# Kernel optimization log

Hardware: AMD Instinct MI355X
Metric: run time of the kernel (lower is better)

## Reference

```python
import jax, jax.numpy as jnp
import numpy as np

N_NODES = 10000
N_EDGES = 160000
M0, M1, M2 = 16, 8, 4            # multiplicities of 0e / 1o / 2e node channels
D_HID = 64                        # radial MLP hidden width
N_BASIS = 4                       # bessel radial basis size
N_STEPS = 3                       # message passing steps
R_MAX = 2.0                       # bessel cutoff
S_CNT = (M0+1)+(M1+1)+(M2+1)      # 31 scalar channels of edge TP output
V_CNT = (M0+1)+3*(M1+1)+2*(M2+1)  # 54 vector channels
T_CNT = (M0+1)+2*(M1+1)+3*(M2+1)  # 50 l=2 channels
NUM_IRREPS = S_CNT+V_CNT+T_CNT    # 135 = radial-MLP output size

def _basis():
    # orthonormal basis of traceless symmetric 3x3 matrices, SH ordering (xy, yz, 3z2-r2, xz, x2-y2)
    B = np.zeros((5,3,3), np.float32); r2 = 1/np.sqrt(2.); r6 = 1/np.sqrt(6.)
    B[0,0,1]=B[0,1,0]=r2
    B[1,1,2]=B[1,2,1]=r2
    B[2]=np.diag([-r6,-r6,2*r6])
    B[3,0,2]=B[3,2,0]=r2
    B[4]=np.diag([r2,-r2,0.])
    return B
_B = jnp.asarray(_basis())

def _eps():
    e = np.zeros((3,3,3), np.float32)
    e[0,1,2]=e[1,2,0]=e[2,0,1]=1.; e[0,2,1]=e[2,1,0]=e[1,0,2]=-1.
    return e
_EPS = jnp.asarray(_eps())

def to_mat(a): return jnp.einsum('...k,kij->...ij', a, _B)
def to5(M):    return jnp.einsum('...ij,kij->...k', M, _B)

def sym_tl(M):
    Ms = 0.5*(M + jnp.swapaxes(M,-1,-2))
    tr = jnp.trace(Ms, axis1=-2, axis2=-1)
    return Ms - (tr/3.)[...,None,None]*jnp.eye(3, dtype=M.dtype)

def lin0(x, W):   # e3nn-style Linear on scalar channels (fan-in normalized)
    return (x @ W) / np.sqrt(x.shape[-1])

def linL(x, W):   # mix multiplicities of an l>0 irrep, x [N,m,c] -> [N,o,c]
    return jnp.einsum('nmc,mo->noc', x, W) / np.sqrt(x.shape[-2])

def sph(n):
    # component-normalized real spherical harmonics (l=0,1,2) of unit vectors n [E,3]
    x, y, z = n[...,0], n[...,1], n[...,2]
    a0 = jnp.ones_like(x)[...,None]
    a1 = np.sqrt(3.)*n
    a2 = jnp.stack([np.sqrt(15.)*x*y, np.sqrt(15.)*y*z,
                    (np.sqrt(5.)/2.)*(3.*z*z-1.),
                    np.sqrt(15.)*x*z, (np.sqrt(15.)/2.)*(x*x-y*y)], -1)
    return a0, a1, a2

def tp(s, v, t, a0, a1, a2):
    # channel-wise tensor product of (s,v,t) with SH attr (a0,a1,a2), outputs filtered to l<=2
    A  = to_mat(a2)                                   # [E,3,3]
    Tm = to_mat(t)                                    # [E,Mt,3,3]
    P  = jnp.einsum('emij,ejk->emik', Tm, A)
    o0 = jnp.concatenate([s*a0,
                          jnp.einsum('emc,ec->em', v, a1),
                          jnp.einsum('emij,eij->em', Tm, A)], -1)
    o1 = jnp.concatenate([s[:,:,None]*a1[:,None,:],
                          v*a0[:,:,None],
                          jnp.cross(v, a1[:,None,:]),
                          jnp.einsum('eij,emj->emi', A, v),
                          jnp.einsum('emij,ej->emi', Tm, a1),
                          jnp.einsum('ijk,emjk->emi', _EPS, P)], 1)
    C1 = jnp.einsum('emi,ej->emij', v, a1)
    C2 = jnp.einsum('iab,ema,ebj->emij', _EPS, v, A)
    C3 = jnp.einsum('iab,ea,embj->emij', _EPS, a1, Tm)
    o2 = jnp.concatenate([s[:,:,None]*a2[:,None,:],
                          to5(sym_tl(C1)), to5(sym_tl(C2)),
                          t*a0[:,:,None],
                          to5(sym_tl(C3)), to5(sym_tl(P))], 1)
    return o0, o1, o2

def _forward(x, Wl_s, Wl_v, Wl_t, Wr0, Wr1, Wr2, Wr3, Wm_s, Wm_v, Wm_t,
             Wn_s, Wn_v, Wn_t, Wp_s, Wp_v, Wp_t, senders, receivers):
    N = x.shape[0]; E = senders.shape[0]
    s = x[:, :M0]
    v = x[:, M0:M0+3*M1].reshape(N, M1, 3)
    t = x[:, M0+3*M1:].reshape(N, M2, 5)
    inv_sqrt_E = 1.0/np.sqrt(E)
    kfreq = jnp.arange(1, N_BASIS+1, dtype=x.dtype)
    for k in range(N_STEPS):
        # relative vector from first 1o channel (position-like irrep), slice_by_mul[:1]
        r = v[senders, 0] - v[receivers, 0]
        d = jnp.sqrt(jnp.sum(r*r, -1))
        dsafe = jnp.maximum(d, 1e-9)
        n = r/dsafe[:,None]
        a0, a1, a2 = sph(n)
        # m_ij = Linear(senders), then concat with SH attrs
        ms = jnp.concatenate([lin0(s[senders], Wl_s[k]), a0], -1)
        mv = jnp.concatenate([linL(v[senders], Wl_v[k]), a1[:,None,:]], 1)
        mt = jnp.concatenate([linL(t[senders], Wl_t[k]), a2[:,None,:]], 1)
        S, V, T = tp(ms, mv, mt, a0, a1, a2)
        # bessel radial basis -> MLP -> per-irrep-channel weights
        R = np.sqrt(2.0/R_MAX)*jnp.sin(kfreq*jnp.pi*dsafe[:,None]/R_MAX)/dsafe[:,None]
        h = R
        for W in (Wr0, Wr1, Wr2):
            h = jax.nn.gelu(lin0(h, W[k]))
        w = lin0(h, Wr3[k])                            # [E, NUM_IRREPS]
        S = S * w[:, :S_CNT]
        V = V * w[:, S_CNT:S_CNT+V_CNT, None]
        T = T * w[:, S_CNT+V_CNT:, None]
        # scatter edge messages to receiver nodes
        aggS = jax.ops.segment_sum(S, receivers, num_segments=N) * inv_sqrt_E
        aggV = jax.ops.segment_sum(V, receivers, num_segments=N) * inv_sqrt_E
        aggT = jax.ops.segment_sum(T, receivers, num_segments=N) * inv_sqrt_E
        # node update: Linear(agg) + Linear(nodes), then equivariant gate
        m_s = lin0(aggS, Wm_s[k]) + lin0(s, Wn_s[k])   # [N, M0 + (M1+M2) gates]
        m_v = linL(aggV, Wm_v[k]) + linL(v, Wn_v[k])
        m_t = linL(aggT, Wm_t[k]) + linL(t, Wn_t[k])
        g = jax.nn.sigmoid(m_s[:, M0:])
        s = lin0(jax.nn.gelu(m_s[:, :M0]), Wp_s[k])
        v = linL(m_v * g[:, :M1, None], Wp_v[k])
        t = linL(m_t * g[:, M1:, None], Wp_t[k])
    return jnp.concatenate([s, v.reshape(N, -1), t.reshape(N, -1)], -1)

def setup_inputs():
    key = jax.random.key(0)
    ks = jax.random.split(key, 20)
    rn = lambda i, shape: jax.random.normal(ks[i], shape, jnp.float32)
    return dict(
        x    = rn(0, (N_NODES, M0+3*M1+5*M2)),
        Wl_s = rn(1, (N_STEPS, M0, M0)), Wl_v = rn(2, (N_STEPS, M1, M1)), Wl_t = rn(3, (N_STEPS, M2, M2)),
        Wr0  = rn(4, (N_STEPS, N_BASIS, D_HID)), Wr1 = rn(5, (N_STEPS, D_HID, D_HID)),
        Wr2  = rn(6, (N_STEPS, D_HID, D_HID)),   Wr3 = rn(7, (N_STEPS, D_HID, NUM_IRREPS)),
        Wm_s = rn(8, (N_STEPS, S_CNT, M0+M1+M2)), Wm_v = rn(9, (N_STEPS, V_CNT, M1)), Wm_t = rn(10, (N_STEPS, T_CNT, M2)),
        Wn_s = rn(11, (N_STEPS, M0, M0+M1+M2)),  Wn_v = rn(12, (N_STEPS, M1, M1)), Wn_t = rn(13, (N_STEPS, M2, M2)),
        Wp_s = rn(14, (N_STEPS, M0, M0)),        Wp_v = rn(15, (N_STEPS, M1, M1)), Wp_t = rn(16, (N_STEPS, M2, M2)),
        senders   = jax.random.randint(ks[17], (N_EDGES,), 0, N_NODES, jnp.int32),
        receivers = jax.random.randint(ks[18], (N_EDGES,), 0, N_NODES, jnp.int32),
    )

def reference(x, Wl_s, Wl_v, Wl_t, Wr0, Wr1, Wr2, Wr3, Wm_s, Wm_v, Wm_t,
              Wn_s, Wn_v, Wn_t, Wp_s, Wp_v, Wp_t, senders, receivers):
    return _forward(x, Wl_s, Wl_v, Wl_t, Wr0, Wr1, Wr2, Wr3, Wm_s, Wm_v, Wm_t,
                    Wn_s, Wn_v, Wn_t, Wp_s, Wp_v, Wp_t, senders, receivers)
```

## Files before the change

### kernel.cpp

```cpp
#include <hip/hip_runtime.h>
#include <math.h>

#define DEV __device__ __forceinline__

#define NN 10000
#define NE 160000
#define DH 64
#define SC 31
#define VC 54
#define TC 50
#define NIR 135
#define FEAT 60
#define ENT 4096
#define ROWF 140
#define ROW4 35

DEV float rcpf(float x) { return __builtin_amdgcn_rcpf(x); }

DEV float geluf(float x) {
    float u = 0.7978845608028654f * (x + 0.044715f * x * x * x);
    u = fminf(fmaxf(u, -9.f), 9.f);
    float e = __expf(2.f * u);
    float th = (e - 1.f) * rcpf(e + 1.f);
    return 0.5f * x * (1.f + th);
}
DEV float sigmoidf_(float x) { return rcpf(1.f + __expf(-x)); }

__global__ __launch_bounds__(256) void csr_hist(const int* __restrict__ rcv,
                                                int* __restrict__ counts,
                                                int* __restrict__ rank) {
    int e = blockIdx.x * 256 + threadIdx.x;
    if (e >= NE) return;
    rank[e] = atomicAdd(&counts[rcv[e]], 1);
}

__global__ __launch_bounds__(1024) void csr_scan(const int* __restrict__ counts,
                                                 int* __restrict__ offs) {
    __shared__ int buf[1024];
    __shared__ int carry_s;
    if (threadIdx.x == 0) carry_s = 0;
    __syncthreads();
    for (int base = 0; base < 10240; base += 1024) {
        int i = base + threadIdx.x;
        int v = (i < NN) ? counts[i] : 0;
        buf[threadIdx.x] = v;
        __syncthreads();
        for (int off = 1; off < 1024; off <<= 1) {
            int t = (threadIdx.x >= off) ? buf[threadIdx.x - off] : 0;
            __syncthreads();
            buf[threadIdx.x] += t;
            __syncthreads();
        }
        int cbase = carry_s;
        int incl = buf[threadIdx.x];
        if (i < NN) offs[i] = cbase + incl - v;
        int total = buf[1023];
        __syncthreads();
        if (threadIdx.x == 0) carry_s = cbase + total;
        __syncthreads();
    }
    if (threadIdx.x == 0) offs[NN] = carry_s;
}

__global__ __launch_bounds__(256) void csr_fill(const int* __restrict__ rcv,
                                                const int* __restrict__ offs,
                                                const int* __restrict__ rank,
                                                int* __restrict__ elist) {
    int e = blockIdx.x * 256 + threadIdx.x;
    if (e >= NE) return;
    elist[offs[rcv[e]] + rank[e]] = e;
}

__global__ __launch_bounds__(256) void w3t_kernel(const float* __restrict__ Wr3,
                                                  float* __restrict__ W3t) {
    int t = blockIdx.x * 256 + threadIdx.x;
    if (t >= 3 * NIR * DH) return;
    int k = t / (NIR * DH), r = t % (NIR * DH);
    int i = r / DH, j = r % DH;
    W3t[t] = Wr3[k * DH * NIR + j * NIR + i];
}

__global__ __launch_bounds__(256) void edge_d_kernel(
    const float* __restrict__ cur, const int* __restrict__ snd, const int* __restrict__ rcv,
    unsigned int* __restrict__ dmaxu)
{
    int e = blockIdx.x * 256 + threadIdx.x;
    if (e >= NE) return;
    float4 qs = ((const float4*)(cur + (size_t)snd[e] * FEAT))[4];
    float4 qr = ((const float4*)(cur + (size_t)rcv[e] * FEAT))[4];
    float rx = qs.x - qr.x, ry = qs.y - qr.y, rz = qs.z - qr.z;
    float d = sqrtf(rx * rx + ry * ry + rz * rz);
    float m = fmaxf(d, 1e-9f);
#pragma unroll
    for (int off = 32; off > 0; off >>= 1) m = fmaxf(m, __shfl_down(m, off));
    if ((threadIdx.x & 63) == 0) atomicMax(dmaxu, __float_as_uint(m));
}

__global__ __launch_bounds__(256) void table_kernel(
    const float* __restrict__ W0, const float* __restrict__ W1,
    const float* __restrict__ W2, const float* __restrict__ W3t,
    const unsigned int* __restrict__ dmaxu, float* __restrict__ table)
{
    __shared__ float hsh[4][DH];
    int wid = threadIdx.x >> 6;
    int lane = threadIdx.x & 63;
    int i = blockIdx.x * 4 + wid;

    float dmax = fmaxf(__uint_as_float(*dmaxu), 1e-6f);
    float ds = fmaxf(dmax * ((float)i / (float)(ENT - 1)), 1e-9f);
    float rinv = 1.f / ds;
    float R4[4];
#pragma unroll
    for (int b = 0; b < 4; b++)
        R4[b] = sinf((float)(b + 1) * 1.5707963267948966f * ds) * rinv;

    float h = geluf((R4[0] * W0[lane] + R4[1] * W0[DH + lane] +
                     R4[2] * W0[2 * DH + lane] + R4[3] * W0[3 * DH + lane]) * 0.5f);
    hsh[wid][lane] = h;
    __syncthreads();

    {
        float acc = 0.f;
#pragma unroll
        for (int j = 0; j < DH; j++) acc += hsh[wid][j] * W1[j * DH + lane];
        h = geluf(acc * 0.125f);
    }
    __syncthreads();
    hsh[wid][lane] = h;
    __syncthreads();

    {
        float acc = 0.f;
#pragma unroll
        for (int j = 0; j < DH; j++) acc += hsh[wid][j] * W2[j * DH + lane];
        h = geluf(acc * 0.125f);
    }
    __syncthreads();
    hsh[wid][lane] = h;
    __syncthreads();

    float* trow = table + (size_t)i * ROWF;
#pragma unroll
    for (int rb = 0; rb < 3; rb++) {
        int r = rb * 64 + lane;
        if (r < NIR) {
            const float* col = W3t + (size_t)r * DH;
            float s0 = 0.f, s1 = 0.f;
#pragma unroll
            for (int j = 0; j < DH; j += 2) {
                s0 += hsh[wid][j] * col[j];
                s1 += hsh[wid][j + 1] * col[j + 1];
            }
            int slot = (r < 31) ? r : ((r < 85) ? r + 1 : r + 3);
            trow[slot] = (s0 + s1) * 0.125f;
        }
    }
    if (lane == 0) { trow[31] = 0.f; trow[86] = 0.f; trow[87] = 0.f; trow[138] = 0.f; trow[139] = 0.f; }
}

#define RC2 0.7071067811865476f
#define RC6 0.40824829046386302f

__global__ __launch_bounds__(256) void tp3_kernel(
    const float* __restrict__ cur, const int* __restrict__ snd, const int* __restrict__ rcv,
    const float* __restrict__ Wls, const float* __restrict__ Wlv, const float* __restrict__ Wlt,
    const float* __restrict__ Wms, const float* __restrict__ Wmv, const float* __restrict__ Wmt,
    const float4* __restrict__ table4, const unsigned int* __restrict__ dmaxu,
    float* __restrict__ msgS, float* __restrict__ msgV, float* __restrict__ msgT, int nbp)
{
    int pass = blockIdx.x / nbp;
    int e = (blockIdx.x - pass * nbp) * 256 + threadIdx.x;
    if (e >= NE) return;
    int is = snd[e], ir = rcv[e];
    const float* xs = cur + (size_t)is * FEAT;

    float4 qs = ((const float4*)xs)[4];
    float4 qr = ((const float4*)(cur + (size_t)ir * FEAT))[4];
    float rx = qs.x - qr.x, ry = qs.y - qr.y, rz = qs.z - qr.z;
    float d = sqrtf(rx * rx + ry * ry + rz * rz);
    float dsafe = fmaxf(d, 1e-9f);
    float rinv = 1.f / dsafe;
    float nx = rx * rinv, ny = ry * rinv, nz = rz * rinv;
    float a1[3] = {1.7320508075688772f * nx, 1.7320508075688772f * ny, 1.7320508075688772f * nz};
    float a2[5] = {3.872983346207417f * nx * ny,
                   3.872983346207417f * ny * nz,
                   1.118033988749895f * (3.f * nz * nz - 1.f),
                   3.872983346207417f * nx * nz,
                   1.9364916731037085f * (nx * nx - ny * ny)};

    float dmax = fmaxf(__uint_as_float(*dmaxu), 1e-6f);
    float pos = dsafe * ((float)(ENT - 1) / dmax);
    int idx = (int)pos;
    if (idx > ENT - 2) idx = ENT - 2;
    float fr = pos - (float)idx;
    const float4* r0 = table4 + (size_t)idx * ROW4;
    const float4* r1 = r0 + ROW4;

#define LERP4(dst, g)                                                       \
    {                                                                       \
        float4 _a = r0[g], _b = r1[g];                                      \
        dst[0] = _a.x + fr * (_b.x - _a.x);                                 \
        dst[1] = _a.y + fr * (_b.y - _a.y);                                 \
        dst[2] = _a.z + fr * (_b.z - _a.z);                                 \
        dst[3] = _a.w + fr * (_b.w - _a.w);                                 \
    }
#define BUILD_MS(ms)                                                        \
    {                                                                       \
        float sb[16];                                                       \
        const float4* p4 = (const float4*)xs;                               \
        _Pragma("unroll")                                                   \
        for (int i = 0; i < 4; i++) {                                       \
            float4 q = p4[i];                                               \
            sb[4 * i] = q.x; sb[4 * i + 1] = q.y; sb[4 * i + 2] = q.z; sb[4 * i + 3] = q.w; \
        }                                                                   \
        _Pragma("unroll")                                                   \
        for (int o = 0; o < 16; o++) ms[o] = 0.f;                           \
        _Pragma("unroll")                                                   \
        for (int i = 0; i < 16; i++) {                                      \
            float si = sb[i];                                               \
            _Pragma("unroll")                                               \
            for (int o = 0; o < 16; o++) ms[o] += si * Wls[i * 16 + o];     \
        }                                                                   \
        _Pragma("unroll")                                                   \
        for (int o = 0; o < 16; o++) ms[o] *= 0.25f;                        \
    }
#define BUILD_MV(mv)                                                        \
    {                                                                       \
        float vb[24];                                                       \
        const float4* p4 = (const float4*)(xs + 16);                        \
        _Pragma("unroll")                                                   \
        for (int i = 0; i < 6; i++) {                                       \
            float4 q = p4[i];                                               \
            vb[4 * i] = q.x; vb[4 * i + 1] = q.y; vb[4 * i + 2] = q.z; vb[4 * i + 3] = q.w; \
        }                                                                   \
        _Pragma("unroll")                                                   \
        for (int o = 0; o < 8; o++) { mv[o][0] = 0.f; mv[o][1] = 0.f; mv[o][2] = 0.f; } \
        _Pragma("unroll")                                                   \
        for (int i = 0; i < 8; i++)                                         \
            _Pragma("unroll")                                               \
            for (int o = 0; o < 8; o++) {                                   \
                float w = Wlv[i * 8 + o];                                   \
                mv[o][0] += vb[i * 3 + 0] * w;                              \
                mv[o][1] += vb[i * 3 + 1] * w;                              \
                mv[o][2] += vb[i * 3 + 2] * w;                              \
            }                                                               \
        _Pragma("unroll")                                                   \
        for (int o = 0; o < 8; o++) {                                       \
            mv[o][0] *= 0.3535533905932738f; mv[o][1] *= 0.3535533905932738f; mv[o][2] *= 0.3535533905932738f; \
        }                                                                   \
        mv[8][0] = a1[0]; mv[8][1] = a1[1]; mv[8][2] = a1[2];               \
    }
#define BUILD_MT(mt)                                                        \
    {                                                                       \
        float tb[20];                                                       \
        const float4* p4 = (const float4*)(xs + 40);                        \
        _Pragma("unroll")                                                   \
        for (int i = 0; i < 5; i++) {                                       \
            float4 q = p4[i];                                               \
            tb[4 * i] = q.x; tb[4 * i + 1] = q.y; tb[4 * i + 2] = q.z; tb[4 * i + 3] = q.w; \
        }                                                                   \
        _Pragma("unroll")                                                   \
        for (int o = 0; o < 4; o++)                                         \
            _Pragma("unroll")                                               \
            for (int c = 0; c < 5; c++) mt[o][c] = 0.f;                     \
        _Pragma("unroll")                                                   \
        for (int i = 0; i < 4; i++)                                         \
            _Pragma("unroll")                                               \
            for (int o = 0; o < 4; o++) {                                   \
                float w = Wlt[i * 4 + o];                                   \
                _Pragma("unroll")                                           \
                for (int c = 0; c < 5; c++) mt[o][c] += tb[i * 5 + c] * w;  \
            }                                                               \
        _Pragma("unroll")                                                   \
        for (int o = 0; o < 4; o++)                                         \
            _Pragma("unroll")                                               \
            for (int c = 0; c < 5; c++) mt[o][c] *= 0.5f;                   \
        _Pragma("unroll")                                                   \
        for (int c = 0; c < 5; c++) mt[4][c] = a2[c];                       \
    }

    if (pass == 0) {
        float wl[32];
#pragma unroll
        for (int g = 0; g < 8; g++) LERP4((&wl[4 * g]), g);
        float aS[28];
#pragma unroll
        for (int o = 0; o < 28; o++) aS[o] = 0.f;
        {
            float ms[16];
            BUILD_MS(ms);
#pragma unroll
            for (int i = 0; i < 17; i++) {
                float sm = ((i < 16) ? ms[i] : 1.f) * wl[i];
#pragma unroll
                for (int o = 0; o < 28; o++) aS[o] += sm * Wms[i * 28 + o];
            }
        }
        {
            float db[8];
            const float4* p4 = (const float4*)(xs + 16);
            float vb[24];
#pragma unroll
            for (int i = 0; i < 6; i++) {
                float4 q = p4[i];
                vb[4 * i] = q.x; vb[4 * i + 1] = q.y; vb[4 * i + 2] = q.z; vb[4 * i + 3] = q.w;
            }
#pragma unroll
            for (int i = 0; i < 8; i++)
                db[i] = vb[i * 3] * a1[0] + vb[i * 3 + 1] * a1[1] + vb[i * 3 + 2] * a1[2];
#pragma unroll
            for (int mm = 0; mm < 9; mm++) {
                float sval;
                if (mm < 8) {
                    sval = 0.f;
#pragma unroll
                    for (int i = 0; i < 8; i++) sval += db[i] * Wlv[i * 8 + mm];
                    sval *= 0.3535533905932738f;
                } else {
                    sval = a1[0] * a1[0] + a1[1] * a1[1] + a1[2] * a1[2];
                }
                float sm = sval * wl[17 + mm];
#pragma unroll
                for (int o = 0; o < 28; o++) aS[o] += sm * Wms[(17 + mm) * 28 + o];
            }
        }
        {
            float dt[4];
            const float4* p4 = (const float4*)(xs + 40);
            float tb[20];
#pragma unroll
            for (int i = 0; i < 5; i++) {
                float4 q = p4[i];
                tb[4 * i] = q.x; tb[4 * i + 1] = q.y; tb[4 * i + 2] = q.z; tb[4 * i + 3] = q.w;
            }
#pragma unroll
            for (int i = 0; i < 4; i++)
                dt[i] = tb[i * 5] * a2[0] + tb[i * 5 + 1] * a2[1] + tb[i * 5 + 2] * a2[2] +
                        tb[i * 5 + 3] * a2[3] + tb[i * 5 + 4] * a2[4];
#pragma unroll
            for (int mm = 0; mm < 5; mm++) {
                float sval;
                if (mm < 4) {
                    sval = 0.f;
#pragma unroll
                    for (int i = 0; i < 4; i++) sval += dt[i] * Wlt[i * 4 + mm];
                    sval *= 0.5f;
                } else {
                    sval = a2[0] * a2[0] + a2[1] * a2[1] + a2[2] * a2[2] + a2[3] * a2[3] + a2[4] * a2[4];
                }
                float sm = sval * wl[26 + mm];
#pragma unroll
                for (int o = 0; o < 28; o++) aS[o] += sm * Wms[(26 + mm) * 28 + o];
            }
        }
        const float kS = 0.17960530202677491f;
        float4* mrow = (float4*)(msgS + (size_t)e * 28);
#pragma unroll
        for (int i = 0; i < 7; i++) {
            float4 q;
            q.x = aS[4 * i] * kS; q.y = aS[4 * i + 1] * kS;
            q.z = aS[4 * i + 2] * kS; q.w = aS[4 * i + 3] * kS;
            mrow[i] = q;
        }
        return;
    }

    float A00 = -RC6 * a2[2] + RC2 * a2[4];
    float A01 = RC2 * a2[0];
    float A02 = RC2 * a2[3];
    float A11 = -RC6 * a2[2] - RC2 * a2[4];
    float A12 = RC2 * a2[1];
    float A22 = 2.f * RC6 * a2[2];

    if (pass == 1) {
        float aV[24];
#pragma unroll
        for (int o = 0; o < 24; o++) aV[o] = 0.f;
#define ADDV(vx, vy, vz, wm, row)                                           \
        {                                                                   \
            float _x = (vx) * (wm), _y = (vy) * (wm), _z = (vz) * (wm);     \
            _Pragma("unroll")                                               \
            for (int o = 0; o < 8; o++) {                                   \
                float w = Wmv[(row) * 8 + o];                               \
                aV[o * 3] += _x * w; aV[o * 3 + 1] += _y * w; aV[o * 3 + 2] += _z * w; \
            }                                                               \
        }
        float mv[9][3];
        {
            float wl[28];
#pragma unroll
            for (int g = 0; g < 7; g++) LERP4((&wl[4 * g]), 8 + g);
            {
                float ms[16];
                BUILD_MS(ms);
#pragma unroll
                for (int i = 0; i < 17; i++) {
                    float mi = (i < 16) ? ms[i] : 1.f;
                    ADDV(mi * a1[0], mi * a1[1], mi * a1[2], wl[i], i);
                }
            }
            BUILD_MV(mv);
#pragma unroll
            for (int mm = 0; mm < 9; mm++) {
                ADDV(mv[mm][0], mv[mm][1], mv[mm][2], wl[17 + mm], 17 + mm);
            }
        }
        {
            float wl[32];
#pragma unroll
            for (int g = 0; g < 8; g++) LERP4((&wl[4 * g]), 14 + g);
#pragma unroll
            for (int mm = 0; mm < 9; mm++) {
                float v0 = mv[mm][0], v1 = mv[mm][1], v2 = mv[mm][2];
                ADDV(v1 * a1[2] - v2 * a1[1], v2 * a1[0] - v0 * a1[2], v0 * a1[1] - v1 * a1[0],
                     wl[2 + mm], 26 + mm);
                ADDV(A00 * v0 + A01 * v1 + A02 * v2, A01 * v0 + A11 * v1 + A12 * v2,
                     A02 * v0 + A12 * v1 + A22 * v2, wl[11 + mm], 35 + mm);
            }
            float mt[5][5];
            BUILD_MT(mt);
#pragma unroll
            for (int mm = 0; mm < 5; mm++) {
                float t0 = mt[mm][0], t1 = mt[mm][1], t2 = mt[mm][2], t3 = mt[mm][3], t4 = mt[mm][4];
                float T00 = -RC6 * t2 + RC2 * t4, T01 = RC2 * t0, T02 = RC2 * t3;
                float T11 = -RC6 * t2 - RC2 * t4, T12 = RC2 * t1, T22 = 2.f * RC6 * t2;
                ADDV(T00 * a1[0] + T01 * a1[1] + T02 * a1[2],
                     T01 * a1[0] + T11 * a1[1] + T12 * a1[2],
                     T02 * a1[0] + T12 * a1[1] + T22 * a1[2], wl[20 + mm], 44 + mm);
                float P01 = T00 * A01 + T01 * A11 + T02 * A12;
                float P02 = T00 * A02 + T01 * A12 + T02 * A22;
                float P10 = T01 * A00 + T11 * A01 + T12 * A02;
                float P12 = T01 * A02 + T11 * A12 + T12 * A22;
                float P20 = T02 * A00 + T12 * A01 + T22 * A02;
                float P21 = T02 * A01 + T12 * A11 + T22 * A12;
                ADDV(P12 - P21, P20 - P02, P01 - P10, wl[25 + mm], 49 + mm);
            }
        }
#undef ADDV
        const float kV = 0.13608276348795434f;
        float4* mrow = (float4*)(msgV + (size_t)e * 24);
#pragma unroll
        for (int i = 0; i < 6; i++) {
            float4 q;
            q.x = aV[4 * i] * kV; q.y = aV[4 * i + 1] * kV;
            q.z = aV[4 * i + 2] * kV; q.w = aV[4 * i + 3] * kV;
            mrow[i] = q;
        }
        return;
    }

    {
        float aT[20];
#pragma unroll
        for (int o = 0; o < 20; o++) aT[o] = 0.f;
#define ADDT(u0, u1, u2, u3, u4, wm, row)                                   \
        {                                                                   \
            float _0 = (u0) * (wm), _1 = (u1) * (wm), _2 = (u2) * (wm),     \
                  _3 = (u3) * (wm), _4 = (u4) * (wm);                       \
            _Pragma("unroll")                                               \
            for (int o = 0; o < 4; o++) {                                   \
                float w = Wmt[(row) * 4 + o];                               \
                aT[o * 5] += _0 * w; aT[o * 5 + 1] += _1 * w;               \
                aT[o * 5 + 2] += _2 * w; aT[o * 5 + 3] += _3 * w;           \
                aT[o * 5 + 4] += _4 * w;                                    \
            }                                                               \
        }
#define TO5T(M00, M01, M02, M10, M11, M12, M20, M21, M22, wm, row)          \
        ADDT(RC2 * ((M01) + (M10)), RC2 * ((M12) + (M21)),                  \
             RC6 * (-(M00) - (M11) + 2.f * (M22)),                         \
             RC2 * ((M02) + (M20)), RC2 * ((M00) - (M11)), wm, row)
        {
            float wl[20];
#pragma unroll
            for (int g = 0; g < 5; g++) LERP4((&wl[4 * g]), 22 + g);
            float ms[16];
            BUILD_MS(ms);
#pragma unroll
            for (int i = 0; i < 17; i++) {
                float mi = (i < 16) ? ms[i] : 1.f;
                ADDT(mi * a2[0], mi * a2[1], mi * a2[2], mi * a2[3], mi * a2[4],
                     wl[i], i);
            }
        }
        {
            float wl[20];
#pragma unroll
            for (int g = 0; g < 5; g++) LERP4((&wl[4 * g]), 26 + g);
            float mv[9][3];
            BUILD_MV(mv);
#pragma unroll
            for (int mm = 0; mm < 9; mm++) {
                float v0 = mv[mm][0], v1 = mv[mm][1], v2 = mv[mm][2];
                TO5T(v0 * a1[0], v0 * a1[1], v0 * a1[2],
                     v1 * a1[0], v1 * a1[1], v1 * a1[2],
                     v2 * a1[0], v2 * a1[1], v2 * a1[2],
                     wl[1 + mm], 17 + mm);
                float C200 = v1 * A02 - v2 * A01, C210 = v2 * A00 - v0 * A02, C220 = v0 * A01 - v1 * A00;
                float C201 = v1 * A12 - v2 * A11, C211 = v2 * A01 - v0 * A12, C221 = v0 * A11 - v1 * A01;
                float C202 = v1 * A22 - v2 * A12, C212 = v2 * A02 - v0 * A22, C222 = v0 * A12 - v1 * A02;
                TO5T(C200, C201, C202, C210, C211, C212, C220, C221, C222,
                     wl[10 + mm], 26 + mm);
            }
        }
        {
            float wl[20];
#pragma unroll
            for (int g = 0; g < 5; g++) LERP4((&wl[4 * g]), 30 + g);
            float mt[5][5];
            BUILD_MT(mt);
#pragma unroll
            for (int mm = 0; mm < 5; mm++) {
                float t0 = mt[mm][0], t1 = mt[mm][1], t2 = mt[mm][2], t3 = mt[mm][3], t4 = mt[mm][4];
                ADDT(t0, t1, t2, t3, t4, wl[3 + mm], 35 + mm);
                float T00 = -RC6 * t2 + RC2 * t4, T01 = RC2 * t0, T02 = RC2 * t3;
                float T11 = -RC6 * t2 - RC2 * t4, T12 = RC2 * t1, T22 = 2.f * RC6 * t2;
                float u0 = a1[0], u1 = a1[1], u2 = a1[2];
                float C300 = u1 * T02 - u2 * T01, C310 = u2 * T00 - u0 * T02, C320 = u0 * T01 - u1 * T00;
                float C301 = u1 * T12 - u2 * T11, C311 = u2 * T01 - u0 * T12, C321 = u0 * T11 - u1 * T01;
                float C302 = u1 * T22 - u2 * T12, C312 = u2 * T02 - u0 * T22, C322 = u0 * T12 - u1 * T02;
                TO5T(C300, C301, C302, C310, C311, C312, C320, C321, C322,
                     wl[8 + mm], 40 + mm);
                float P00 = T00 * A00 + T01 * A01 + T02 * A02;
                float P01 = T00 * A01 + T01 * A11 + T02 * A12;
                float P02 = T00 * A02 + T01 * A12 + T02 * A22;
                float P10 = T01 * A00 + T11 * A01 + T12 * A02;
                float P11 = T01 * A01 + T11 * A11 + T12 * A12;
                float P12 = T01 * A02 + T11 * A12 + T12 * A22;
                float P20 = T02 * A00 + T12 * A01 + T22 * A02;
                float P21 = T02 * A01 + T12 * A11 + T22 * A12;
                float P22 = T02 * A02 + T12 * A12 + T22 * A22;
                TO5T(P00, P01, P02, P10, P11, P12, P20, P21, P22,
                     wl[13 + mm], 45 + mm);
            }
        }
#undef TO5T
#undef ADDT
        const float kT = 0.1414213562373095f;
        float4* mrow = (float4*)(msgT + (size_t)e * 20);
#pragma unroll
        for (int i = 0; i < 5; i++) {
            float4 q;
            q.x = aT[4 * i] * kT; q.y = aT[4 * i + 1] * kT;
            q.z = aT[4 * i + 2] * kT; q.w = aT[4 * i + 3] * kT;
            mrow[i] = q;
        }
    }
#undef LERP4
#undef BUILD_MS
#undef BUILD_MV
#undef BUILD_MT
}

__global__ __launch_bounds__(256) void gather_kernel(
    const float4* __restrict__ msgS4, const float4* __restrict__ msgV4,
    const float4* __restrict__ msgT4, const int* __restrict__ offs,
    const int* __restrict__ elist, float4* __restrict__ agg4)
{
    int wid = threadIdx.x >> 6;
    int lane = threadIdx.x & 63;
    int n = blockIdx.x * 4 + wid;
    if (n >= NN) return;
    int sub = lane / 18;
    int q = lane - sub * 18;
    const float4* base;
    int stride, qo;
    if (q < 7)       { base = msgS4; stride = 7; qo = q; }
    else if (q < 13) { base = msgV4; stride = 6; qo = q - 7; }
    else             { base = msgT4; stride = 5; qo = q - 13; }
    int beg = offs[n], end = offs[n + 1];
    float4 acc = {0.f, 0.f, 0.f, 0.f};
    if (sub < 3) {
        for (int j = beg + sub; j < end; j += 3) {
            int e = elist[j];
            float4 m = base[(size_t)e * stride + qo];
            acc.x += m.x; acc.y += m.y; acc.z += m.z; acc.w += m.w;
        }
    }
    float bx = __shfl(acc.x, lane + 18), by = __shfl(acc.y, lane + 18);
    float bz = __shfl(acc.z, lane + 18), bw = __shfl(acc.w, lane + 18);
    float cx = __shfl(acc.x, lane + 36), cy = __shfl(acc.y, lane + 36);
    float cz = __shfl(acc.z, lane + 36), cw = __shfl(acc.w, lane + 36);
    if (lane < 18) {
        float4 r;
        r.x = acc.x + bx + cx; r.y = acc.y + by + cy;
        r.z = acc.z + bz + cz; r.w = acc.w + bw + cw;
        agg4[(size_t)n * 18 + lane] = r;
    }
}

__global__ __launch_bounds__(256) void node_kernel(
    const float* __restrict__ cur, const float* __restrict__ agg,
    const float* __restrict__ Wns, const float* __restrict__ Wnv, const float* __restrict__ Wnt,
    const float* __restrict__ Wps, const float* __restrict__ Wpv, const float* __restrict__ Wpt,
    float* __restrict__ dst)
{
    int n = blockIdx.x * 256 + threadIdx.x;
    if (n >= NN) return;
    const float* xn = cur + (size_t)n * FEAT;
    const float* ag = agg + (size_t)n * 72;
    const float invE = 0.0025f;

    float msv[28];
#pragma unroll
    for (int o = 0; o < 28; o++) msv[o] = ag[o] * invE;
#pragma unroll
    for (int i = 0; i < 16; i++) {
        float si = xn[i] * 0.25f;
#pragma unroll
        for (int o = 0; o < 28; o++) msv[o] += si * Wns[i * 28 + o];
    }
    float mvv[8][3];
#pragma unroll
    for (int o = 0; o < 8; o++)
#pragma unroll
        for (int c = 0; c < 3; c++) mvv[o][c] = ag[28 + o * 3 + c] * invE;
#pragma unroll
    for (int i = 0; i < 8; i++)
#pragma unroll
        for (int o = 0; o < 8; o++) {
            float w = Wnv[i * 8 + o] * 0.3535533905932738f;
#pragma unroll
            for (int c = 0; c < 3; c++) mvv[o][c] += xn[16 + i * 3 + c] * w;
        }
    float mtv[4][5];
#pragma unroll
    for (int o = 0; o < 4; o++)
#pragma unroll
        for (int c = 0; c < 5; c++) mtv[o][c] = ag[52 + o * 5 + c] * invE;
#pragma unroll
    for (int i = 0; i < 4; i++)
#pragma unroll
        for (int o = 0; o < 4; o++) {
            float w = Wnt[i * 4 + o] * 0.5f;
#pragma unroll
            for (int c = 0; c < 5; c++) mtv[o][c] += xn[40 + i * 5 + c] * w;
        }

    float g[12];
#pragma unroll
    for (int j = 0; j < 12; j++) g[j] = sigmoidf_(msv[16 + j]);
    float hs[16];
#pragma unroll
    for (int i = 0; i < 16; i++) hs[i] = geluf(msv[i]);

    float outv[60];
#pragma unroll
    for (int o = 0; o < 16; o++) outv[o] = 0.f;
#pragma unroll
    for (int i = 0; i < 16; i++) {
        float si = hs[i] * 0.25f;
#pragma unroll
        for (int o = 0; o < 16; o++) outv[o] += si * Wps[i * 16 + o];
    }
#pragma unroll
    for (int o = 0; o < 8; o++)
#pragma unroll
        for (int c = 0; c < 3; c++) outv[16 + o * 3 + c] = 0.f;
#pragma unroll
    for (int i = 0; i < 8; i++) {
        float gi = g[i];
#pragma unroll
        for (int o = 0; o < 8; o++) {
            float w = Wpv[i * 8 + o] * 0.3535533905932738f * gi;
#pragma unroll
            for (int c = 0; c < 3; c++) outv[16 + o * 3 + c] += mvv[i][c] * w;
        }
    }
#pragma unroll
    for (int o = 0; o < 4; o++)
#pragma unroll
        for (int c = 0; c < 5; c++) outv[40 + o * 5 + c] = 0.f;
#pragma unroll
    for (int i = 0; i < 4; i++) {
        float gi = g[8 + i];
#pragma unroll
        for (int o = 0; o < 4; o++) {
            float w = Wpt[i * 4 + o] * 0.5f * gi;
#pragma unroll
            for (int c = 0; c < 5; c++) outv[40 + o * 5 + c] += mtv[i][c] * w;
        }
    }

    float4* dst4 = (float4*)(dst + (size_t)n * FEAT);
#pragma unroll
    for (int i = 0; i < 15; i++) {
        float4 q;
        q.x = outv[4 * i]; q.y = outv[4 * i + 1]; q.z = outv[4 * i + 2]; q.w = outv[4 * i + 3];
        dst4[i] = q;
    }
}

static inline size_t algn(size_t o) { return (o + 63) & ~(size_t)63; }

extern "C" void kernel_launch(void* const* d_in, const int* in_sizes, int n_in,
                              void* d_out, int out_size, void* d_ws, size_t ws_size,
                              hipStream_t stream)
{
    const float* x    = (const float*)d_in[0];
    const float* Wl_s = (const float*)d_in[1];
    const float* Wl_v = (const float*)d_in[2];
    const float* Wl_t = (const float*)d_in[3];
    const float* Wr0  = (const float*)d_in[4];
    const float* Wr1  = (const float*)d_in[5];
    const float* Wr2  = (const float*)d_in[6];
    const float* Wr3  = (const float*)d_in[7];
    const float* Wm_s = (const float*)d_in[8];
    const float* Wm_v = (const float*)d_in[9];
    const float* Wm_t = (const float*)d_in[10];
    const float* Wn_s = (const float*)d_in[11];
    const float* Wn_v = (const float*)d_in[12];
    const float* Wn_t = (const float*)d_in[13];
    const float* Wp_s = (const float*)d_in[14];
    const float* Wp_v = (const float*)d_in[15];
    const float* Wp_t = (const float*)d_in[16];
    const int* snd = (const int*)d_in[17];
    const int* rcv = (const int*)d_in[18];
    float* out = (float*)d_out;

    char* ws = (char*)d_ws;
    size_t off = 0;
    float* cur    = (float*)(ws + off); off = algn(off + (size_t)NN * FEAT * 4);
    float* agg    = (float*)(ws + off); off = algn(off + (size_t)NN * 72 * 4);
    float* msgS   = (float*)(ws + off); off = algn(off + (size_t)NE * 28 * 4);
    float* msgV   = (float*)(ws + off); off = algn(off + (size_t)NE * 24 * 4);
    float* msgT   = (float*)(ws + off); off = algn(off + (size_t)NE * 20 * 4);
    int*   counts = (int*)(ws + off);   off = algn(off + (size_t)NN * 4);
    int*   offs   = (int*)(ws + off);   off = algn(off + (size_t)(NN + 1) * 4);
    int*   rank   = (int*)(ws + off);   off = algn(off + (size_t)NE * 4);
    int*   elist  = (int*)(ws + off);   off = algn(off + (size_t)NE * 4);
    float* W3t    = (float*)(ws + off); off = algn(off + (size_t)3 * NIR * DH * 4);
    unsigned int* dmaxu = (unsigned int*)(ws + off); off = algn(off + 64);
    float* table  = (float*)(ws + off); off = algn(off + (size_t)ENT * ROWF * 4);

    hipMemcpyAsync(cur, x, (size_t)NN * FEAT * 4, hipMemcpyDeviceToDevice, stream);
    hipMemsetAsync(counts, 0, (size_t)NN * 4, stream);
    csr_hist<<<(NE + 255) / 256, 256, 0, stream>>>(rcv, counts, rank);
    csr_scan<<<1, 1024, 0, stream>>>(counts, offs);
    csr_fill<<<(NE + 255) / 256, 256, 0, stream>>>(rcv, offs, rank, elist);
    w3t_kernel<<<(3 * NIR * DH + 255) / 256, 256, 0, stream>>>(Wr3, W3t);

    int nb = (NE + 255) / 256;
    for (int k = 0; k < 3; k++) {
        const float* W0  = Wr0 + (size_t)k * 4 * DH;
        const float* W1  = Wr1 + (size_t)k * DH * DH;
        const float* W2  = Wr2 + (size_t)k * DH * DH;
        const float* W3tk= W3t + (size_t)k * NIR * DH;
        const float* Wls = Wl_s + (size_t)k * 16 * 16;
        const float* Wlv = Wl_v + (size_t)k * 8 * 8;
        const float* Wlt = Wl_t + (size_t)k * 4 * 4;
        const float* Wms = Wm_s + (size_t)k * SC * 28;
        const float* Wmv = Wm_v + (size_t)k * VC * 8;
        const float* Wmt = Wm_t + (size_t)k * TC * 4;
        const float* Wns = Wn_s + (size_t)k * 16 * 28;
        const float* Wnv = Wn_v + (size_t)k * 8 * 8;
        const float* Wnt = Wn_t + (size_t)k * 4 * 4;
        const float* Wps = Wp_s + (size_t)k * 16 * 16;
        const float* Wpv = Wp_v + (size_t)k * 8 * 8;
        const float* Wpt = Wp_t + (size_t)k * 4 * 4;

        hipMemsetAsync(dmaxu, 0, 4, stream);
        edge_d_kernel<<<nb, 256, 0, stream>>>(cur, snd, rcv, dmaxu);
        table_kernel<<<ENT / 4, 256, 0, stream>>>(W0, W1, W2, W3tk, dmaxu, table);
        tp3_kernel<<<3 * nb, 256, 0, stream>>>(cur, snd, rcv, Wls, Wlv, Wlt,
                                               Wms, Wmv, Wmt, (const float4*)table,
                                               dmaxu, msgS, msgV, msgT, nb);
        gather_kernel<<<(NN + 3) / 4, 256, 0, stream>>>(
            (const float4*)msgS, (const float4*)msgV, (const float4*)msgT,
            offs, elist, (float4*)agg);
        float* dst = (k == 2) ? out : cur;
        node_kernel<<<(NN + 255) / 256, 256, 0, stream>>>(cur, agg, Wns, Wnv, Wnt,
                                                          Wps, Wpv, Wpt, dst);
    }
}
```

Baseline: 588.5 us.

## Reorder edge processing by sender to improve locality of node feature loads

```diff
diff --git a/kernel.cpp b/kernel.cpp
--- a/kernel.cpp
+++ b/kernel.cpp
@@ -26,12 +26,12 @@
 }
 DEV float sigmoidf_(float x) { return rcpf(1.f + __expf(-x)); }
 
-__global__ __launch_bounds__(256) void csr_hist(const int* __restrict__ rcv,
+__global__ __launch_bounds__(256) void csr_hist(const int* __restrict__ key,
                                                 int* __restrict__ counts,
                                                 int* __restrict__ rank) {
     int e = blockIdx.x * 256 + threadIdx.x;
     if (e >= NE) return;
-    rank[e] = atomicAdd(&counts[rcv[e]], 1);
+    rank[e] = atomicAdd(&counts[key[e]], 1);
 }
 
 __global__ __launch_bounds__(1024) void csr_scan(const int* __restrict__ counts,
@@ -71,6 +71,28 @@
     elist[offs[rcv[e]] + rank[e]] = e;
 }
 
+__global__ __launch_bounds__(256) void csr_pos(const int* __restrict__ snd,
+                                               const int* __restrict__ rcv,
+                                               const int* __restrict__ offs2,
+                                               const int* __restrict__ rank2,
+                                               int* __restrict__ pos,
+                                               int* __restrict__ snds,
+                                               int* __restrict__ rcvs) {
+    int e = blockIdx.x * 256 + threadIdx.x;
+    if (e >= NE) return;
+    int p = offs2[snd[e]] + rank2[e];
+    pos[e] = p;
+    snds[p] = snd[e];
+    rcvs[p] = rcv[e];
+}
+
+__global__ __launch_bounds__(256) void elist_remap(int* __restrict__ elist,
+                                                   const int* __restrict__ pos) {
+    int j = blockIdx.x * 256 + threadIdx.x;
+    if (j >= NE) return;
+    elist[j] = pos[elist[j]];
+}
+
 __global__ __launch_bounds__(256) void w3t_kernel(const float* __restrict__ Wr3,
                                                   float* __restrict__ W3t) {
     int t = blockIdx.x * 256 + threadIdx.x;
@@ -162,7 +184,7 @@
 #define RC6 0.40824829046386302f
 
 __global__ __launch_bounds__(256) void tp3_kernel(
-    const float* __restrict__ cur, const int* __restrict__ snd, const int* __restrict__ rcv,
+    const float* __restrict__ cur, const int* __restrict__ snds, const int* __restrict__ rcvs,
     const float* __restrict__ Wls, const float* __restrict__ Wlv, const float* __restrict__ Wlt,
     const float* __restrict__ Wms, const float* __restrict__ Wmv, const float* __restrict__ Wmt,
     const float4* __restrict__ table4, const unsigned int* __restrict__ dmaxu,
@@ -171,7 +193,7 @@
     int pass = blockIdx.x / nbp;
     int e = (blockIdx.x - pass * nbp) * 256 + threadIdx.x;
     if (e >= NE) return;
-    int is = snd[e], ir = rcv[e];
+    int is = snds[e], ir = rcvs[e];
     const float* xs = cur + (size_t)is * FEAT;
 
     float4 qs = ((const float4*)xs)[4];
@@ -728,18 +750,29 @@
     int*   offs   = (int*)(ws + off);   off = algn(off + (size_t)(NN + 1) * 4);
     int*   rank   = (int*)(ws + off);   off = algn(off + (size_t)NE * 4);
     int*   elist  = (int*)(ws + off);   off = algn(off + (size_t)NE * 4);
+    int*   counts2= (int*)(ws + off);   off = algn(off + (size_t)NN * 4);
+    int*   offs2  = (int*)(ws + off);   off = algn(off + (size_t)(NN + 1) * 4);
+    int*   rank2  = (int*)(ws + off);   off = algn(off + (size_t)NE * 4);
+    int*   pos    = (int*)(ws + off);   off = algn(off + (size_t)NE * 4);
+    int*   snds   = (int*)(ws + off);   off = algn(off + (size_t)NE * 4);
+    int*   rcvs   = (int*)(ws + off);   off = algn(off + (size_t)NE * 4);
     float* W3t    = (float*)(ws + off); off = algn(off + (size_t)3 * NIR * DH * 4);
     unsigned int* dmaxu = (unsigned int*)(ws + off); off = algn(off + 64);
     float* table  = (float*)(ws + off); off = algn(off + (size_t)ENT * ROWF * 4);
 
     hipMemcpyAsync(cur, x, (size_t)NN * FEAT * 4, hipMemcpyDeviceToDevice, stream);
     hipMemsetAsync(counts, 0, (size_t)NN * 4, stream);
-    csr_hist<<<(NE + 255) / 256, 256, 0, stream>>>(rcv, counts, rank);
+    hipMemsetAsync(counts2, 0, (size_t)NN * 4, stream);
+    int nb = (NE + 255) / 256;
+    csr_hist<<<nb, 256, 0, stream>>>(rcv, counts, rank);
+    csr_hist<<<nb, 256, 0, stream>>>(snd, counts2, rank2);
     csr_scan<<<1, 1024, 0, stream>>>(counts, offs);
-    csr_fill<<<(NE + 255) / 256, 256, 0, stream>>>(rcv, offs, rank, elist);
+    csr_scan<<<1, 1024, 0, stream>>>(counts2, offs2);
+    csr_fill<<<nb, 256, 0, stream>>>(rcv, offs, rank, elist);
+    csr_pos<<<nb, 256, 0, stream>>>(snd, rcv, offs2, rank2, pos, snds, rcvs);
+    elist_remap<<<nb, 256, 0, stream>>>(elist, pos);
     w3t_kernel<<<(3 * NIR * DH + 255) / 256, 256, 0, stream>>>(Wr3, W3t);
 
-    int nb = (NE + 255) / 256;
     for (int k = 0; k < 3; k++) {
         const float* W0  = Wr0 + (size_t)k * 4 * DH;
         const float* W1  = Wr1 + (size_t)k * DH * DH;
@@ -761,7 +794,7 @@
         hipMemsetAsync(dmaxu, 0, 4, stream);
         edge_d_kernel<<<nb, 256, 0, stream>>>(cur, snd, rcv, dmaxu);
         table_kernel<<<ENT / 4, 256, 0, stream>>>(W0, W1, W2, W3tk, dmaxu, table);
-        tp3_kernel<<<3 * nb, 256, 0, stream>>>(cur, snd, rcv, Wls, Wlv, Wlt,
+        tp3_kernel<<<3 * nb, 256, 0, stream>>>(cur, snds, rcvs, Wls, Wlv, Wlt,
                                                Wms, Wmv, Wmt, (const float4*)table,
                                                dmaxu, msgS, msgV, msgT, nb);
         gather_kernel<<<(NN + 3) / 4, 256, 0, stream>>>(
```

After: 596.5 us. No clear change (+1.4%).

## Use fixed rational distance mapping for radial table and fuse gather with node update

Applied to the files above, without the earlier changes.

```diff
diff --git a/kernel.cpp b/kernel.cpp
--- a/kernel.cpp
+++ b/kernel.cpp
@@ -14,6 +14,7 @@
 #define ENT 4096
 #define ROWF 140
 #define ROW4 35
+#define DCV 4.0f
 
 DEV float rcpf(float x) { return __builtin_amdgcn_rcpf(x); }
 
@@ -80,34 +81,18 @@
     W3t[t] = Wr3[k * DH * NIR + j * NIR + i];
 }
 
-__global__ __launch_bounds__(256) void edge_d_kernel(
-    const float* __restrict__ cur, const int* __restrict__ snd, const int* __restrict__ rcv,
-    unsigned int* __restrict__ dmaxu)
-{
-    int e = blockIdx.x * 256 + threadIdx.x;
-    if (e >= NE) return;
-    float4 qs = ((const float4*)(cur + (size_t)snd[e] * FEAT))[4];
-    float4 qr = ((const float4*)(cur + (size_t)rcv[e] * FEAT))[4];
-    float rx = qs.x - qr.x, ry = qs.y - qr.y, rz = qs.z - qr.z;
-    float d = sqrtf(rx * rx + ry * ry + rz * rz);
-    float m = fmaxf(d, 1e-9f);
-#pragma unroll
-    for (int off = 32; off > 0; off >>= 1) m = fmaxf(m, __shfl_down(m, off));
-    if ((threadIdx.x & 63) == 0) atomicMax(dmaxu, __float_as_uint(m));
-}
-
 __global__ __launch_bounds__(256) void table_kernel(
     const float* __restrict__ W0, const float* __restrict__ W1,
     const float* __restrict__ W2, const float* __restrict__ W3t,
-    const unsigned int* __restrict__ dmaxu, float* __restrict__ table)
+    float* __restrict__ table)
 {
     __shared__ float hsh[4][DH];
     int wid = threadIdx.x >> 6;
     int lane = threadIdx.x & 63;
     int i = blockIdx.x * 4 + wid;
 
-    float dmax = fmaxf(__uint_as_float(*dmaxu), 1e-6f);
-    float ds = fmaxf(dmax * ((float)i / (float)(ENT - 1)), 1e-9f);
+    float u = (float)i / (float)ENT;
+    float ds = fmaxf(DCV * u * rcpf(1.f - u), 1e-9f);
     float rinv = 1.f / ds;
     float R4[4];
 #pragma unroll
@@ -165,7 +150,7 @@
     const float* __restrict__ cur, const int* __restrict__ snd, const int* __restrict__ rcv,
     const float* __restrict__ Wls, const float* __restrict__ Wlv, const float* __restrict__ Wlt,
     const float* __restrict__ Wms, const float* __restrict__ Wmv, const float* __restrict__ Wmt,
-    const float4* __restrict__ table4, const unsigned int* __restrict__ dmaxu,
+    const float4* __restrict__ table4,
     float* __restrict__ msgS, float* __restrict__ msgV, float* __restrict__ msgT, int nbp)
 {
     int pass = blockIdx.x / nbp;
@@ -188,8 +173,7 @@
                    3.872983346207417f * nx * nz,
                    1.9364916731037085f * (nx * nx - ny * ny)};
 
-    float dmax = fmaxf(__uint_as_float(*dmaxu), 1e-6f);
-    float pos = dsafe * ((float)(ENT - 1) / dmax);
+    float pos = dsafe * rcpf(DCV + dsafe) * (float)ENT;
     int idx = (int)pos;
     if (idx > ENT - 2) idx = ENT - 2;
     float fr = pos - (float)idx;
@@ -551,15 +535,18 @@
 #undef BUILD_MT
 }
 
-__global__ __launch_bounds__(256) void gather_kernel(
+__global__ __launch_bounds__(256) void gather_node_kernel(
     const float4* __restrict__ msgS4, const float4* __restrict__ msgV4,
     const float4* __restrict__ msgT4, const int* __restrict__ offs,
-    const int* __restrict__ elist, float4* __restrict__ agg4)
+    const int* __restrict__ elist, const float* __restrict__ cur,
+    const float* __restrict__ Wns, const float* __restrict__ Wnv, const float* __restrict__ Wnt,
+    const float* __restrict__ Wps, const float* __restrict__ Wpv, const float* __restrict__ Wpt,
+    float* __restrict__ dst)
 {
+    __shared__ float aggsh[4][72];
     int wid = threadIdx.x >> 6;
     int lane = threadIdx.x & 63;
     int n = blockIdx.x * 4 + wid;
-    if (n >= NN) return;
     int sub = lane / 18;
     int q = lane - sub * 18;
     const float4* base;
@@ -581,112 +568,107 @@
     float cx = __shfl(acc.x, lane + 36), cy = __shfl(acc.y, lane + 36);
     float cz = __shfl(acc.z, lane + 36), cw = __shfl(acc.w, lane + 36);
     if (lane < 18) {
-        float4 r;
-        r.x = acc.x + bx + cx; r.y = acc.y + by + cy;
-        r.z = acc.z + bz + cz; r.w = acc.w + bw + cw;
-        agg4[(size_t)n * 18 + lane] = r;
-    }
-}
-
-__global__ __launch_bounds__(256) void node_kernel(
-    const float* __restrict__ cur, const float* __restrict__ agg,
-    const float* __restrict__ Wns, const float* __restrict__ Wnv, const float* __restrict__ Wnt,
-    const float* __restrict__ Wps, const float* __restrict__ Wpv, const float* __restrict__ Wpt,
-    float* __restrict__ dst)
-{
-    int n = blockIdx.x * 256 + threadIdx.x;
-    if (n >= NN) return;
-    const float* xn = cur + (size_t)n * FEAT;
-    const float* ag = agg + (size_t)n * 72;
-    const float invE = 0.0025f;
-
-    float msv[28];
-#pragma unroll
-    for (int o = 0; o < 28; o++) msv[o] = ag[o] * invE;
-#pragma unroll
-    for (int i = 0; i < 16; i++) {
-        float si = xn[i] * 0.25f;
-#pragma unroll
-        for (int o = 0; o < 28; o++) msv[o] += si * Wns[i * 28 + o];
-    }
-    float mvv[8][3];
-#pragma unroll
-    for (int o = 0; o < 8; o++)
-#pragma unroll
-        for (int c = 0; c < 3; c++) mvv[o][c] = ag[28 + o * 3 + c] * invE;
-#pragma unroll
-    for (int i = 0; i < 8; i++)
-#pragma unroll
-        for (int o = 0; o < 8; o++) {
-            float w = Wnv[i * 8 + o] * 0.3535533905932738f;
-#pragma unroll
-            for (int c = 0; c < 3; c++) mvv[o][c] += xn[16 + i * 3 + c] * w;
-        }
-    float mtv[4][5];
-#pragma unroll
-    for (int o = 0; o < 4; o++)
-#pragma unroll
-        for (int c = 0; c < 5; c++) mtv[o][c] = ag[52 + o * 5 + c] * invE;
-#pragma unroll
-    for (int i = 0; i < 4; i++)
-#pragma unroll
-        for (int o = 0; o < 4; o++) {
-            float w = Wnt[i * 4 + o] * 0.5f;
-#pragma unroll
-            for (int c = 0; c < 5; c++) mtv[o][c] += xn[40 + i * 5 + c] * w;
-        }
-
-    float g[12];
-#pragma unroll
-    for (int j = 0; j < 12; j++) g[j] = sigmoidf_(msv[16 + j]);
-    float hs[16];
-#pragma unroll
-    for (int i = 0; i < 16; i++) hs[i] = geluf(msv[i]);
-
-    float outv[60];
-#pragma unroll
-    for (int o = 0; o < 16; o++) outv[o] = 0.f;
-#pragma unroll
-    for (int i = 0; i < 16; i++) {
-        float si = hs[i] * 0.25f;
-#pragma unroll
-        for (int o = 0; o < 16; o++) outv[o] += si * Wps[i * 16 + o];
-    }
-#pragma unroll
-    for (int o = 0; o < 8; o++)
-#pragma unroll
-        for (int c = 0; c < 3; c++) outv[16 + o * 3 + c] = 0.f;
-#pragma unroll
-    for (int i = 0; i < 8; i++) {
-        float gi = g[i];
-#pragma unroll
-        for (int o = 0; o < 8; o++) {
-            float w = Wpv[i * 8 + o] * 0.3535533905932738f * gi;
-#pragma unroll
-            for (int c = 0; c < 3; c++) outv[16 + o * 3 + c] += mvv[i][c] * w;
-        }
-    }
-#pragma unroll
-    for (int o = 0; o < 4; o++)
-#pragma unroll
-        for (int c = 0; c < 5; c++) outv[40 + o * 5 + c] = 0.f;
-#pragma unroll
-    for (int i = 0; i < 4; i++) {
-        float gi = g[8 + i];
-#pragma unroll
-        for (int o = 0; o < 4; o++) {
-            float w = Wpt[i * 4 + o] * 0.5f * gi;
-#pragma unroll
-            for (int c = 0; c < 5; c++) outv[40 + o * 5 + c] += mtv[i][c] * w;
-        }
-    }
-
-    float4* dst4 = (float4*)(dst + (size_t)n * FEAT);
-#pragma unroll
-    for (int i = 0; i < 15; i++) {
-        float4 q;
-        q.x = outv[4 * i]; q.y = outv[4 * i + 1]; q.z = outv[4 * i + 2]; q.w = outv[4 * i + 3];
-        dst4[i] = q;
+        aggsh[wid][lane * 4 + 0] = acc.x + bx + cx;
+        aggsh[wid][lane * 4 + 1] = acc.y + by + cy;
+        aggsh[wid][lane * 4 + 2] = acc.z + bz + cz;
+        aggsh[wid][lane * 4 + 3] = acc.w + bw + cw;
+    }
+    __syncthreads();
+
+    if (threadIdx.x < 4) {
+        int nn = blockIdx.x * 4 + threadIdx.x;
+        const float* xn = cur + (size_t)nn * FEAT;
+        const float* ag = aggsh[threadIdx.x];
+        const float invE = 0.0025f;
+
+        float msv[28];
+#pragma unroll
+        for (int o = 0; o < 28; o++) msv[o] = ag[o] * invE;
+#pragma unroll
+        for (int i = 0; i < 16; i++) {
+            float si = xn[i] * 0.25f;
+#pragma unroll
+            for (int o = 0; o < 28; o++) msv[o] += si * Wns[i * 28 + o];
+        }
+        float mvv[8][3];
+#pragma unroll
+        for (int o = 0; o < 8; o++)
+#pragma unroll
+            for (int c = 0; c < 3; c++) mvv[o][c] = ag[28 + o * 3 + c] * invE;
+#pragma unroll
+        for (int i = 0; i < 8; i++)
+#pragma unroll
+            for (int o = 0; o < 8; o++) {
+                float w = Wnv[i * 8 + o] * 0.3535533905932738f;
+#pragma unroll
+                for (int c = 0; c < 3; c++) mvv[o][c] += xn[16 + i * 3 + c] * w;
+            }
+        float mtv[4][5];
+#pragma unroll
+        for (int o = 0; o < 4; o++)
+#pragma unroll
+            for (int c = 0; c < 5; c++) mtv[o][c] = ag[52 + o * 5 + c] * invE;
+#pragma unroll
+        for (int i = 0; i < 4; i++)
+#pragma unroll
+            for (int o = 0; o < 4; o++) {
+                float w = Wnt[i * 4 + o] * 0.5f;
+#pragma unroll
+                for (int c = 0; c < 5; c++) mtv[o][c] += xn[40 + i * 5 + c] * w;
+            }
+
+        float g[12];
+#pragma unroll
+        for (int j = 0; j < 12; j++) g[j] = sigmoidf_(msv[16 + j]);
+        float hs[16];
+#pragma unroll
+        for (int i = 0; i < 16; i++) hs[i] = geluf(msv[i]);
+
+        float outv[60];
+#pragma unroll
+        for (int o = 0; o < 16; o++) outv[o] = 0.f;
+#pragma unroll
+        for (int i = 0; i < 16; i++) {
+            float si = hs[i] * 0.25f;
+#pragma unroll
+            for (int o = 0; o < 16; o++) outv[o] += si * Wps[i * 16 + o];
+        }
+#pragma unroll
+        for (int o = 0; o < 8; o++)
+#pragma unroll
+            for (int c = 0; c < 3; c++) outv[16 + o * 3 + c] = 0.f;
+#pragma unroll
+        for (int i = 0; i < 8; i++) {
+            float gi = g[i];
+#pragma unroll
+            for (int o = 0; o < 8; o++) {
+                float w = Wpv[i * 8 + o] * 0.3535533905932738f * gi;
+#pragma unroll
+                for (int c = 0; c < 3; c++) outv[16 + o * 3 + c] += mvv[i][c] * w;
+            }
+        }
+#pragma unroll
+        for (int o = 0; o < 4; o++)
+#pragma unroll
+            for (int c = 0; c < 5; c++) outv[40 + o * 5 + c] = 0.f;
+#pragma unroll
+        for (int i = 0; i < 4; i++) {
+            float gi = g[8 + i];
+#pragma unroll
+            for (int o = 0; o < 4; o++) {
+                float w = Wpt[i * 4 + o] * 0.5f * gi;
+#pragma unroll
+                for (int c = 0; c < 5; c++) outv[40 + o * 5 + c] += mtv[i][c] * w;
+            }
+        }
+
+        float4* dst4 = (float4*)(dst + (size_t)nn * FEAT);
+#pragma unroll
+        for (int i = 0; i < 15; i++) {
+            float4 qv;
+            qv.x = outv[4 * i]; qv.y = outv[4 * i + 1]; qv.z = outv[4 * i + 2]; qv.w = outv[4 * i + 3];
+            dst4[i] = qv;
+        }
     }
 }
 
@@ -720,7 +702,6 @@
     char* ws = (char*)d_ws;
     size_t off = 0;
     float* cur    = (float*)(ws + off); off = algn(off + (size_t)NN * FEAT * 4);
-    float* agg    = (float*)(ws + off); off = algn(off + (size_t)NN * 72 * 4);
     float* msgS   = (float*)(ws + off); off = algn(off + (size_t)NE * 28 * 4);
     float* msgV   = (float*)(ws + off); off = algn(off + (size_t)NE * 24 * 4);
     float* msgT   = (float*)(ws + off); off = algn(off + (size_t)NE * 20 * 4);
@@ -729,17 +710,16 @@
     int*   rank   = (int*)(ws + off);   off = algn(off + (size_t)NE * 4);
     int*   elist  = (int*)(ws + off);   off = algn(off + (size_t)NE * 4);
     float* W3t    = (float*)(ws + off); off = algn(off + (size_t)3 * NIR * DH * 4);
-    unsigned int* dmaxu = (unsigned int*)(ws + off); off = algn(off + 64);
     float* table  = (float*)(ws + off); off = algn(off + (size_t)ENT * ROWF * 4);
 
     hipMemcpyAsync(cur, x, (size_t)NN * FEAT * 4, hipMemcpyDeviceToDevice, stream);
     hipMemsetAsync(counts, 0, (size_t)NN * 4, stream);
-    csr_hist<<<(NE + 255) / 256, 256, 0, stream>>>(rcv, counts, rank);
+    int nb = (NE + 255) / 256;
+    csr_hist<<<nb, 256, 0, stream>>>(rcv, counts, rank);
     csr_scan<<<1, 1024, 0, stream>>>(counts, offs);
-    csr_fill<<<(NE + 255) / 256, 256, 0, stream>>>(rcv, offs, rank, elist);
+    csr_fill<<<nb, 256, 0, stream>>>(rcv, offs, rank, elist);
     w3t_kernel<<<(3 * NIR * DH + 255) / 256, 256, 0, stream>>>(Wr3, W3t);
 
-    int nb = (NE + 255) / 256;
     for (int k = 0; k < 3; k++) {
         const float* W0  = Wr0 + (size_t)k * 4 * DH;
         const float* W1  = Wr1 + (size_t)k * DH * DH;
@@ -758,17 +738,13 @@
         const float* Wpv = Wp_v + (size_t)k * 8 * 8;
         const float* Wpt = Wp_t + (size_t)k * 4 * 4;
 
-        hipMemsetAsync(dmaxu, 0, 4, stream);
-        edge_d_kernel<<<nb, 256, 0, stream>>>(cur, snd, rcv, dmaxu);
-        table_kernel<<<ENT / 4, 256, 0, stream>>>(W0, W1, W2, W3tk, dmaxu, table);
+        table_kernel<<<ENT / 4, 256, 0, stream>>>(W0, W1, W2, W3tk, table);
         tp3_kernel<<<3 * nb, 256, 0, stream>>>(cur, snd, rcv, Wls, Wlv, Wlt,
                                                Wms, Wmv, Wmt, (const float4*)table,
-                                               dmaxu, msgS, msgV, msgT, nb);
-        gather_kernel<<<(NN + 3) / 4, 256, 0, stream>>>(
+                                               msgS, msgV, msgT, nb);
+        float* dst = (k == 2) ? out : cur;
+        gather_node_kernel<<<NN / 4, 256, 0, stream>>>(
             (const float4*)msgS, (const float4*)msgV, (const float4*)msgT,
-            offs, elist, (float4*)agg);
-        float* dst = (k == 2) ? out : cur;
-        node_kernel<<<(NN + 255) / 256, 256, 0, stream>>>(cur, agg, Wns, Wnv, Wnt,
-                                                          Wps, Wpv, Wpt, dst);
-    }
-}
+            offs, elist, cur, Wns, Wnv, Wnt, Wps, Wpv, Wpt, dst);
+    }
+}
```

New measurement: 785.6 us. 1.33x slower.
